# Kernel optimization log

Hardware: AMD Instinct MI355X
Metric: run time of the kernel (lower is better)

Reference implementation:

```python
import jax, jax.numpy as jnp
import numpy as np

B, T, C = 4, 2048, 2048
H, S = 32, 64
LN_EPS = 1e-5


def _layer_norm(x, w, b):
    mu = jnp.mean(x, axis=-1, keepdims=True)
    var = jnp.mean((x - mu) ** 2, axis=-1, keepdims=True)
    return (x - mu) / jnp.sqrt(var + LN_EPS) * w + b


def setup_inputs() -> dict:
    key = jax.random.key(0)
    ks = jax.random.split(key, 8)
    sc = 1.0 / np.sqrt(C)
    sc4 = 1.0 / np.sqrt(4 * C)
    return {
        "x": jax.random.normal(ks[0], (B, T, C), jnp.float32),
        "time_decay": jnp.full((H, S), -5.0, jnp.float32),
        "time_first": jnp.zeros((H, S), jnp.float32),
        "Wk": jax.random.normal(ks[1], (C, C), jnp.float32) * sc,
        "Wv": jax.random.normal(ks[2], (C, C), jnp.float32) * sc,
        "Wr": jax.random.normal(ks[3], (C, C), jnp.float32) * sc,
        "Wo": jax.random.normal(ks[4], (C, C), jnp.float32) * sc,
        "Wfk": jax.random.normal(ks[5], (C, 4 * C), jnp.float32) * sc,
        "Wfv": jax.random.normal(ks[6], (4 * C, C), jnp.float32) * sc4,
        "ln1_w": jnp.ones((C,), jnp.float32),
        "ln1_b": jnp.zeros((C,), jnp.float32),
        "ln2_w": jnp.ones((C,), jnp.float32),
        "ln2_b": jnp.zeros((C,), jnp.float32),
    }


def reference(x, time_decay, time_first, Wk, Wv, Wr, Wo, Wfk, Wfv,
              ln1_w, ln1_b, ln2_w, ln2_b):
    b, t, c = x.shape
    h, s = time_decay.shape
    xl = _layer_norm(x, ln1_w, ln1_b)
    k = (xl @ Wk).reshape(b, t, h, s)  # [B,T,H,S]
    v = (xl @ Wv).reshape(b, t, h, s)
    r = (xl @ Wr).reshape(b, t, h, s)

    decay = jnp.exp(-jnp.exp(time_decay))  # [H,S]
    u = jnp.exp(k) * v                      # [B,T,H,S]
    u_t = jnp.swapaxes(u, 0, 1)             # [T,B,H,S]

    def step(state, ut):
        state = decay * state + ut
        return state, state

    _, states = jax.lax.scan(step, jnp.zeros((b, h, s), x.dtype), u_t)  # [T,B,H,S]
    # t=0 bonus term: exp(time_first) * v_0 added to wkv only (not the state)
    states = states.at[0].add(jnp.exp(time_first) * v[:, 0])
    wkv = jnp.swapaxes(states, 0, 1)        # [B,T,H,S]

    rwkv = jax.nn.sigmoid(r) * wkv
    x = x + rwkv.reshape(b, t, c) @ Wo
    xl2 = _layer_norm(x, ln2_w, ln2_b)
    ffn = (jax.nn.relu(xl2 @ Wfk) ** 2) @ Wfv
    return x + ffn
```

## Files before the change

kernel.cpp:

```cpp
#include <hip/hip_runtime.h>
#include <hip/hip_bf16.h>
#include <stdint.h>

#define B_  4
#define T_  2048
#define C_  2048
#define H_  32
#define S_  64
#define M_  (B_ * T_)
#define C4_ (4 * C_)
#define C2_ (2 * C_)
#define LN_EPS 1e-5f
#define NCH 16
#define CLEN 128
#define NCHAN (B_ * C_)

typedef unsigned short u16;
typedef __attribute__((ext_vector_type(8))) short short8;
typedef __attribute__((ext_vector_type(4))) float f32x4;

__device__ __forceinline__ u16 f2bf(float f) {
  uint32_t u = __float_as_uint(f);
  u = (u + 0x7FFFu + ((u >> 16) & 1u)) >> 16;
  return (u16)u;
}
__device__ __forceinline__ float bf2f(u16 u) {
  return __uint_as_float(((uint32_t)u) << 16);
}

__device__ __forceinline__ void gload_lds16(const void* g, void* l) {
  __builtin_amdgcn_global_load_lds(
      (const __attribute__((address_space(1))) uint32_t*)g,
      (__attribute__((address_space(3))) uint32_t*)l, 16, 0, 0);
}

__global__ __launch_bounds__(256) void k_transpose_cast(
    const float* __restrict__ in, u16* __restrict__ out, int ld, int R, int Cn) {
  __shared__ float tile[32][33];
  const int tx = threadIdx.x & 31, ty = threadIdx.x >> 5;
  const int c0 = blockIdx.x * 32, r0 = blockIdx.y * 32;
#pragma unroll
  for (int i = 0; i < 4; ++i) {
    int r = ty + i * 8;
    tile[r][tx] = in[(size_t)(r0 + r) * ld + (c0 + tx)];
  }
  __syncthreads();
#pragma unroll
  for (int i = 0; i < 4; ++i) {
    int cc = ty + i * 8;
    out[(size_t)(c0 + cc) * R + (r0 + tx)] = f2bf(tile[tx][cc]);
  }
}

__global__ __launch_bounds__(256) void k_layernorm_bf16(
    const float* __restrict__ x, const float* __restrict__ w,
    const float* __restrict__ bias, u16* __restrict__ out) {
  const int row = blockIdx.x;
  const int t = threadIdx.x;
  const float* xr = x + (size_t)row * C_;
  float4 a = ((const float4*)xr)[2 * t];
  float4 b = ((const float4*)xr)[2 * t + 1];
  float s = a.x + a.y + a.z + a.w + b.x + b.y + b.z + b.w;
  float q = a.x * a.x + a.y * a.y + a.z * a.z + a.w * a.w +
            b.x * b.x + b.y * b.y + b.z * b.z + b.w * b.w;
#pragma unroll
  for (int off = 32; off > 0; off >>= 1) {
    s += __shfl_down(s, off);
    q += __shfl_down(q, off);
  }
  __shared__ float rs[8];
  const int wv = t >> 6;
  if ((t & 63) == 0) { rs[wv] = s; rs[4 + wv] = q; }
  __syncthreads();
  s = rs[0] + rs[1] + rs[2] + rs[3];
  q = rs[4] + rs[5] + rs[6] + rs[7];
  const float mean = s * (1.0f / C_);
  const float rstd = rsqrtf(q * (1.0f / C_) - mean * mean + LN_EPS);
  float4 w0 = ((const float4*)w)[2 * t], w1 = ((const float4*)w)[2 * t + 1];
  float4 b0 = ((const float4*)bias)[2 * t], b1 = ((const float4*)bias)[2 * t + 1];
  uint4 pk;
  pk.x = (uint32_t)f2bf((a.x - mean) * rstd * w0.x + b0.x) |
         ((uint32_t)f2bf((a.y - mean) * rstd * w0.y + b0.y) << 16);
  pk.y = (uint32_t)f2bf((a.z - mean) * rstd * w0.z + b0.z) |
         ((uint32_t)f2bf((a.w - mean) * rstd * w0.w + b0.w) << 16);
  pk.z = (uint32_t)f2bf((b.x - mean) * rstd * w1.x + b1.x) |
         ((uint32_t)f2bf((b.y - mean) * rstd * w1.y + b1.y) << 16);
  pk.w = (uint32_t)f2bf((b.z - mean) * rstd * w1.z + b1.z) |
         ((uint32_t)f2bf((b.w - mean) * rstd * w1.w + b1.w) << 16);
  ((uint4*)(out + (size_t)row * C_))[t] = pk;
}

__device__ __forceinline__ void stage_half(
    const u16* __restrict__ G, int ldK, int row0, int kcol0,
    u16* lds_half, int tid) {
#pragma unroll
  for (int i = 0; i < 2; ++i) {
    const int slot = i * 512 + tid;
    const int row = slot >> 2;
    const int gs = slot & 3;
    const int gsrc = gs ^ ((row >> 1) & 3);
    gload_lds16(G + (size_t)(row0 + row) * ldK + kcol0 + gsrc * 8,
                ((char*)lds_half) + i * 8192 + (tid >> 6) * 1024);
  }
}

__device__ __forceinline__ short8 frag(const u16* half_base, int row, int g0) {
  const int g = g0 ^ ((row >> 1) & 3);
  return *(const short8*)(half_base + row * 32 + g * 8);
}

template <int EPI>
__global__ __launch_bounds__(512, 2) void k_gemm8(
    const u16* __restrict__ A, const u16* __restrict__ Bt,
    void* __restrict__ Out, const float* __restrict__ Res,
    int M, int N, int K) {
  __shared__ u16 As[2][2][256 * 32];
  __shared__ u16 Bs[2][2][256 * 32];
  const int tid = threadIdx.x;
  const int wv = tid >> 6, ln = tid & 63;
  const int wm = wv >> 2, wn = wv & 3;
  const int l15 = ln & 15, g0 = ln >> 4;

  const int lin = blockIdx.y * gridDim.x + blockIdx.x;
  const int xcd = lin & 7, slot = lin >> 3;
  const int bx = slot % gridDim.x;
  const int by = xcd * (gridDim.y >> 3) + slot / gridDim.x;
  const int bm0 = by * 256, bn0 = bx * 256;
  const int NT = K >> 6;

  f32x4 acc[8][4];
#pragma unroll
  for (int m = 0; m < 8; ++m)
#pragma unroll
    for (int n = 0; n < 4; ++n) acc[m][n] = (f32x4)0.0f;

  stage_half(A, K, bm0, 0, &As[0][0][0], tid);
  stage_half(Bt, K, bn0, 0, &Bs[0][0][0], tid);
  stage_half(A, K, bm0, 32, &As[0][1][0], tid);
  stage_half(Bt, K, bn0, 32, &Bs[0][1][0], tid);
  asm volatile("s_waitcnt vmcnt(4)" ::: "memory");
  __builtin_amdgcn_s_barrier();
  __builtin_amdgcn_sched_barrier(0);

  for (int t = 0; t < NT; ++t) {
    const int c = t & 1, nb = c ^ 1;
    const int kn = (t + 1) << 6;
    const bool stage_on = (t + 1 < NT);
    const bool lastt = (t + 1 == NT);
    short8 bfr[4], af[4];

#pragma unroll
    for (int h = 0; h < 2; ++h) {
#pragma unroll
      for (int n = 0; n < 4; ++n)
        bfr[n] = frag(&Bs[c][h][0], wn * 64 + n * 16 + l15, g0);
#pragma unroll
      for (int m = 0; m < 4; ++m)
        af[m] = frag(&As[c][h][0], wm * 128 + m * 16 + l15, g0);
      if (stage_on) stage_half(A, K, bm0, kn + h * 32, &As[nb][h][0], tid);
#pragma unroll
      for (int m = 0; m < 4; ++m)
#pragma unroll
        for (int n = 0; n < 4; ++n)
          acc[m][n] = __builtin_amdgcn_mfma_f32_16x16x32_bf16(af[m], bfr[n], acc[m][n], 0, 0, 0);

#pragma unroll
      for (int m = 0; m < 4; ++m)
        af[m] = frag(&As[c][h][0], wm * 128 + 64 + m * 16 + l15, g0);
      if (stage_on) stage_half(Bt, K, bn0, kn + h * 32, &Bs[nb][h][0], tid);
#pragma unroll
      for (int m = 0; m < 4; ++m)
#pragma unroll
        for (int n = 0; n < 4; ++n)
          acc[4 + m][n] = __builtin_amdgcn_mfma_f32_16x16x32_bf16(af[m], bfr[n], acc[4 + m][n], 0, 0, 0);

      if (h == 0) {
        if (!lastt) asm volatile("s_waitcnt vmcnt(4)" ::: "memory");
        else        asm volatile("s_waitcnt vmcnt(0)" ::: "memory");
        __builtin_amdgcn_s_barrier();
        __builtin_amdgcn_sched_barrier(0);
      } else if (!lastt) {
        asm volatile("s_waitcnt vmcnt(4)" ::: "memory");
        __builtin_amdgcn_s_barrier();
        __builtin_amdgcn_sched_barrier(0);
      }
    }
  }

#pragma unroll
  for (int m = 0; m < 8; ++m) {
    const int r_base = bm0 + wm * 128 + m * 16 + (ln >> 4) * 4;
#pragma unroll
    for (int n = 0; n < 4; ++n) {
      const int cidx = bn0 + wn * 64 + n * 16 + l15;
#pragma unroll
      for (int i = 0; i < 4; ++i) {
        const size_t off = (size_t)(r_base + i) * N + cidx;
        const float v = acc[m][n][i];
        if constexpr (EPI == 0) {
          ((float*)Out)[off] = v;
        } else if constexpr (EPI == 1) {
          ((float*)Out)[off] = Res[off] + v;
        } else if constexpr (EPI == 2) {
          ((u16*)Out)[off] = f2bf(v);
        } else if constexpr (EPI == 3) {
          const float tpos = v > 0.0f ? v : 0.0f;
          ((u16*)Out)[off] = f2bf(tpos * tpos);
        } else {
          ((float*)Out)[off] += v;
        }
      }
    }
  }
}

__global__ __launch_bounds__(256) void k_scan_a(
    const float* __restrict__ kk, const u16* __restrict__ vv,
    const float* __restrict__ td, float* __restrict__ Sloc) {
  const int g = blockIdx.x * 256 + threadIdx.x;
  const int j = blockIdx.y;
  const int ch = g & (C_ - 1);
  const float d = __expf(-__expf(td[ch]));
  const size_t base = ((size_t)(g >> 11) * T_ + (size_t)j * CLEN) * C_ + ch;
  float s = 0.0f;
#pragma unroll 4
  for (int t = 0; t < CLEN; ++t) {
    const size_t idx = base + (size_t)t * C_;
    s = d * s + __expf(kk[idx]) * bf2f(vv[idx]);
  }
  Sloc[(size_t)j * NCHAN + g] = s;
}

__global__ __launch_bounds__(256) void k_scan_b(
    const float* __restrict__ td, const float* __restrict__ Sloc,
    float* __restrict__ carry) {
  const int g = blockIdx.x * 256 + threadIdx.x;
  const int ch = g & (C_ - 1);
  const float dL = __expf(-__expf(td[ch]) * (float)CLEN);
  float s = 0.0f;
#pragma unroll
  for (int j = 0; j < NCH; ++j) {
    carry[(size_t)j * NCHAN + g] = s;
    s = dL * s + Sloc[(size_t)j * NCHAN + g];
  }
}

__global__ __launch_bounds__(256) void k_scan_c(
    const float* __restrict__ kk, const u16* __restrict__ vv,
    const u16* __restrict__ rr, const float* __restrict__ td,
    const float* __restrict__ tf, const float* __restrict__ carry,
    u16* __restrict__ rwkv) {
  const int g = blockIdx.x * 256 + threadIdx.x;
  const int j = blockIdx.y;
  const int ch = g & (C_ - 1);
  const float d = __expf(-__expf(td[ch]));
  const float bonus = __expf(tf[ch]);
  const size_t base = ((size_t)(g >> 11) * T_ + (size_t)j * CLEN) * C_ + ch;
  float s = carry[(size_t)j * NCHAN + g];
#pragma unroll 2
  for (int t = 0; t < CLEN; ++t) {
    const size_t idx = base + (size_t)t * C_;
    const float vval = bf2f(vv[idx]);
    s = d * s + __expf(kk[idx]) * vval;
    float wkv = s;
    if (j == 0 && t == 0) wkv += bonus * vval;
    const float rv = bf2f(rr[idx]);
    const float sg = 1.0f / (1.0f + __expf(-rv));
    rwkv[idx] = f2bf(sg * wkv);
  }
}

extern "C" void kernel_launch(void* const* d_in, const int* in_sizes, int n_in,
                              void* d_out, int out_size, void* d_ws, size_t ws_size,
                              hipStream_t stream) {
  const float* x    = (const float*)d_in[0];
  const float* td   = (const float*)d_in[1];
  const float* tf   = (const float*)d_in[2];
  const float* Wk   = (const float*)d_in[3];
  const float* Wv   = (const float*)d_in[4];
  const float* Wr   = (const float*)d_in[5];
  const float* Wo   = (const float*)d_in[6];
  const float* Wfk  = (const float*)d_in[7];
  const float* Wfv  = (const float*)d_in[8];
  const float* ln1w = (const float*)d_in[9];
  const float* ln1b = (const float*)d_in[10];
  const float* ln2w = (const float*)d_in[11];
  const float* ln2b = (const float*)d_in[12];
  float* out = (float*)d_out;

  char* p = (char*)d_ws;
  auto alloc = [&](size_t bytes) {
    char* r = p;
    p += (bytes + 255) & ~(size_t)255;
    return r;
  };
  u16*   wbuf = (u16*)alloc((size_t)C_ * C_ * 2);
  u16*   xl   = (u16*)alloc((size_t)M_ * C_ * 2);
  float* kbuf = (float*)alloc((size_t)M_ * C_ * 4);
  u16*   vbuf = (u16*)alloc((size_t)M_ * C_ * 2);
  u16*   rbuf = (u16*)alloc((size_t)M_ * C_ * 2);
  float* Sloc = (float*)alloc((size_t)NCH * NCHAN * 4);
  float* carry = (float*)alloc((size_t)NCH * NCHAN * 4);
  u16* rwkv = rbuf;
  u16* hchunk = xl;
  u16* wfbuf = rbuf;

  const dim3 tgrid(C_ / 32, C_ / 32);
  const dim3 ggrid(C_ / 256, M_ / 256);

  k_layernorm_bf16<<<M_, 256, 0, stream>>>(x, ln1w, ln1b, xl);

  k_transpose_cast<<<tgrid, 256, 0, stream>>>(Wk, wbuf, C_, C_, C_);
  k_gemm8<0><<<ggrid, 512, 0, stream>>>(xl, wbuf, kbuf, nullptr, M_, C_, C_);
  k_transpose_cast<<<tgrid, 256, 0, stream>>>(Wv, wbuf, C_, C_, C_);
  k_gemm8<2><<<ggrid, 512, 0, stream>>>(xl, wbuf, vbuf, nullptr, M_, C_, C_);
  k_transpose_cast<<<tgrid, 256, 0, stream>>>(Wr, wbuf, C_, C_, C_);
  k_gemm8<2><<<ggrid, 512, 0, stream>>>(xl, wbuf, rbuf, nullptr, M_, C_, C_);

  k_scan_a<<<dim3(NCHAN / 256, NCH), 256, 0, stream>>>(kbuf, vbuf, td, Sloc);
  k_scan_b<<<dim3(NCHAN / 256), 256, 0, stream>>>(td, Sloc, carry);
  k_scan_c<<<dim3(NCHAN / 256, NCH), 256, 0, stream>>>(kbuf, vbuf, rbuf, td, tf, carry, rwkv);

  k_transpose_cast<<<tgrid, 256, 0, stream>>>(Wo, wbuf, C_, C_, C_);
  k_gemm8<1><<<ggrid, 512, 0, stream>>>(rwkv, wbuf, out, x, M_, C_, C_);

  u16* xl2 = vbuf;
  k_layernorm_bf16<<<M_, 256, 0, stream>>>(out, ln2w, ln2b, xl2);

  for (int c = 0; c < 2; ++c) {
    k_transpose_cast<<<dim3(C2_ / 32, C_ / 32), 256, 0, stream>>>(
        Wfk + (size_t)c * C2_, wfbuf, C4_, C_, C2_);
    k_gemm8<3><<<dim3(C2_ / 256, M_ / 256), 512, 0, stream>>>(
        xl2, wfbuf, hchunk, nullptr, M_, C2_, C_);
    k_transpose_cast<<<dim3(C_ / 32, C2_ / 32), 256, 0, stream>>>(
        Wfv + (size_t)c * C2_ * C_, wfbuf, C_, C2_, C_);
    k_gemm8<4><<<dim3(C_ / 256, M_ / 256), 512, 0, stream>>>(
        hchunk, wfbuf, out, nullptr, M_, C_, C2_);
  }
}
```

Baseline: 955.6 us.

## Shrink GEMM tile to 256x128 with K=32 steps and higher occupancy

Replaces the 256x256, K-64 double-buffered GEMM with a 256x128 tile that steps K by 32, uses 4x4 accumulators per wave, and requests 4 blocks per CU. This cuts LDS and register use so more blocks can be resident and latency is hidden by occupancy rather than intra-block pipelining. In exchange each tile has lower arithmetic intensity, there is a full barrier with vmcnt(0) every 32-wide K step, and the grid doubles in size.

```diff
diff --git a/kernel.cpp b/kernel.cpp
--- a/kernel.cpp
+++ b/kernel.cpp
@@ -90,106 +90,91 @@
   ((uint4*)(out + (size_t)row * C_))[t] = pk;
 }
 
-__device__ __forceinline__ void stage_half(
-    const u16* __restrict__ G, int ldK, int row0, int kcol0,
-    u16* lds_half, int tid) {
-#pragma unroll
-  for (int i = 0; i < 2; ++i) {
-    const int slot = i * 512 + tid;
-    const int row = slot >> 2;
-    const int gs = slot & 3;
-    const int gsrc = gs ^ ((row >> 1) & 3);
-    gload_lds16(G + (size_t)(row0 + row) * ldK + kcol0 + gsrc * 8,
-                ((char*)lds_half) + i * 8192 + (tid >> 6) * 1024);
-  }
-}
-
-__device__ __forceinline__ short8 frag(const u16* half_base, int row, int g0) {
+__device__ __forceinline__ short8 frag(const u16* buf_base, int row, int g0) {
   const int g = g0 ^ ((row >> 1) & 3);
-  return *(const short8*)(half_base + row * 32 + g * 8);
+  return *(const short8*)(buf_base + row * 32 + g * 8);
 }
 
 template <int EPI>
-__global__ __launch_bounds__(512, 2) void k_gemm8(
+__global__ __launch_bounds__(512, 4) void k_gemm2(
     const u16* __restrict__ A, const u16* __restrict__ Bt,
     void* __restrict__ Out, const float* __restrict__ Res,
     int M, int N, int K) {
-  __shared__ u16 As[2][2][256 * 32];
-  __shared__ u16 Bs[2][2][256 * 32];
+  __shared__ u16 As[2][256 * 32];
+  __shared__ u16 Bs[2][128 * 32];
   const int tid = threadIdx.x;
   const int wv = tid >> 6, ln = tid & 63;
-  const int wm = wv >> 2, wn = wv & 3;
+  const int wm = wv >> 1, wn = wv & 1;
   const int l15 = ln & 15, g0 = ln >> 4;
 
   const int lin = blockIdx.y * gridDim.x + blockIdx.x;
   const int xcd = lin & 7, slot = lin >> 3;
   const int bx = slot % gridDim.x;
   const int by = xcd * (gridDim.y >> 3) + slot / gridDim.x;
-  const int bm0 = by * 256, bn0 = bx * 256;
-  const int NT = K >> 6;
-
-  f32x4 acc[8][4];
-#pragma unroll
-  for (int m = 0; m < 8; ++m)
+  const int bm0 = by * 256, bn0 = bx * 128;
+  const int NT = K >> 5;
+
+  const int arow = tid >> 2, ag = tid & 3;
+  const int agsrc0 = ag ^ ((arow >> 1) & 3);
+  const int agsrc1 = ag ^ (((arow + 128) >> 1) & 3);
+  const int brow = tid >> 2, bg = tid & 3;
+  const int bgsrc = bg ^ ((brow >> 1) & 3);
+
+  f32x4 acc[4][4];
+#pragma unroll
+  for (int m = 0; m < 4; ++m)
 #pragma unroll
     for (int n = 0; n < 4; ++n) acc[m][n] = (f32x4)0.0f;
 
-  stage_half(A, K, bm0, 0, &As[0][0][0], tid);
-  stage_half(Bt, K, bn0, 0, &Bs[0][0][0], tid);
-  stage_half(A, K, bm0, 32, &As[0][1][0], tid);
-  stage_half(Bt, K, bn0, 32, &Bs[0][1][0], tid);
-  asm volatile("s_waitcnt vmcnt(4)" ::: "memory");
+  gload_lds16(A + (size_t)(bm0 + arow) * K + agsrc0 * 8,
+              ((char*)&As[0][0]) + wv * 1024);
+  gload_lds16(A + (size_t)(bm0 + 128 + arow) * K + agsrc1 * 8,
+              ((char*)&As[0][0]) + 8192 + wv * 1024);
+  gload_lds16(Bt + (size_t)(bn0 + brow) * K + bgsrc * 8,
+              ((char*)&Bs[0][0]) + wv * 1024);
+  asm volatile("s_waitcnt vmcnt(0)" ::: "memory");
   __builtin_amdgcn_s_barrier();
   __builtin_amdgcn_sched_barrier(0);
 
   for (int t = 0; t < NT; ++t) {
     const int c = t & 1, nb = c ^ 1;
-    const int kn = (t + 1) << 6;
+    const int kn = (t + 1) << 5;
     const bool stage_on = (t + 1 < NT);
-    const bool lastt = (t + 1 == NT);
-    short8 bfr[4], af[4];
-
-#pragma unroll
-    for (int h = 0; h < 2; ++h) {
+    short8 af[4], bfr[4];
+
+#pragma unroll
+    for (int m = 0; m < 4; ++m)
+      af[m] = frag(&As[c][0], wm * 64 + m * 16 + l15, g0);
+#pragma unroll
+    for (int n = 0; n < 4; ++n)
+      bfr[n] = frag(&Bs[c][0], wn * 64 + n * 16 + l15, g0);
+
+    if (stage_on) {
+      gload_lds16(A + (size_t)(bm0 + arow) * K + kn + agsrc0 * 8,
+                  ((char*)&As[nb][0]) + wv * 1024);
+      gload_lds16(A + (size_t)(bm0 + 128 + arow) * K + kn + agsrc1 * 8,
+                  ((char*)&As[nb][0]) + 8192 + wv * 1024);
+      gload_lds16(Bt + (size_t)(bn0 + brow) * K + kn + bgsrc * 8,
+                  ((char*)&Bs[nb][0]) + wv * 1024);
+    }
+
+#pragma unroll
+    for (int m = 0; m < 4; ++m)
 #pragma unroll
       for (int n = 0; n < 4; ++n)
-        bfr[n] = frag(&Bs[c][h][0], wn * 64 + n * 16 + l15, g0);
-#pragma unroll
-      for (int m = 0; m < 4; ++m)
-        af[m] = frag(&As[c][h][0], wm * 128 + m * 16 + l15, g0);
-      if (stage_on) stage_half(A, K, bm0, kn + h * 32, &As[nb][h][0], tid);
-#pragma unroll
-      for (int m = 0; m < 4; ++m)
-#pragma unroll
-        for (int n = 0; n < 4; ++n)
-          acc[m][n] = __builtin_amdgcn_mfma_f32_16x16x32_bf16(af[m], bfr[n], acc[m][n], 0, 0, 0);
-
-#pragma unroll
-      for (int m = 0; m < 4; ++m)
-        af[m] = frag(&As[c][h][0], wm * 128 + 64 + m * 16 + l15, g0);
-      if (stage_on) stage_half(Bt, K, bn0, kn + h * 32, &Bs[nb][h][0], tid);
-#pragma unroll
-      for (int m = 0; m < 4; ++m)
-#pragma unroll
-        for (int n = 0; n < 4; ++n)
-          acc[4 + m][n] = __builtin_amdgcn_mfma_f32_16x16x32_bf16(af[m], bfr[n], acc[4 + m][n], 0, 0, 0);
-
-      if (h == 0) {
-        if (!lastt) asm volatile("s_waitcnt vmcnt(4)" ::: "memory");
-        else        asm volatile("s_waitcnt vmcnt(0)" ::: "memory");
-        __builtin_amdgcn_s_barrier();
-        __builtin_amdgcn_sched_barrier(0);
-      } else if (!lastt) {
-        asm volatile("s_waitcnt vmcnt(4)" ::: "memory");
-        __builtin_amdgcn_s_barrier();
-        __builtin_amdgcn_sched_barrier(0);
-      }
+        acc[m][n] = __builtin_amdgcn_mfma_f32_16x16x32_bf16(af[m], bfr[n], acc[m][n], 0, 0, 0);
+
+    if (stage_on) {
+      __builtin_amdgcn_sched_barrier(0);
+      asm volatile("s_waitcnt vmcnt(0) lgkmcnt(0)" ::: "memory");
+      __builtin_amdgcn_s_barrier();
+      __builtin_amdgcn_sched_barrier(0);
     }
   }
 
 #pragma unroll
-  for (int m = 0; m < 8; ++m) {
-    const int r_base = bm0 + wm * 128 + m * 16 + (ln >> 4) * 4;
+  for (int m = 0; m < 4; ++m) {
+    const int r_base = bm0 + wm * 64 + m * 16 + g0 * 4;
 #pragma unroll
     for (int n = 0; n < 4; ++n) {
       const int cidx = bn0 + wn * 64 + n * 16 + l15;
@@ -306,23 +291,23 @@
   u16* wfbuf = rbuf;
 
   const dim3 tgrid(C_ / 32, C_ / 32);
-  const dim3 ggrid(C_ / 256, M_ / 256);
+  const dim3 ggrid(C_ / 128, M_ / 256);
 
   k_layernorm_bf16<<<M_, 256, 0, stream>>>(x, ln1w, ln1b, xl);
 
   k_transpose_cast<<<tgrid, 256, 0, stream>>>(Wk, wbuf, C_, C_, C_);
-  k_gemm8<0><<<ggrid, 512, 0, stream>>>(xl, wbuf, kbuf, nullptr, M_, C_, C_);
+  k_gemm2<0><<<ggrid, 512, 0, stream>>>(xl, wbuf, kbuf, nullptr, M_, C_, C_);
   k_transpose_cast<<<tgrid, 256, 0, stream>>>(Wv, wbuf, C_, C_, C_);
-  k_gemm8<2><<<ggrid, 512, 0, stream>>>(xl, wbuf, vbuf, nullptr, M_, C_, C_);
+  k_gemm2<2><<<ggrid, 512, 0, stream>>>(xl, wbuf, vbuf, nullptr, M_, C_, C_);
   k_transpose_cast<<<tgrid, 256, 0, stream>>>(Wr, wbuf, C_, C_, C_);
-  k_gemm8<2><<<ggrid, 512, 0, stream>>>(xl, wbuf, rbuf, nullptr, M_, C_, C_);
+  k_gemm2<2><<<ggrid, 512, 0, stream>>>(xl, wbuf, rbuf, nullptr, M_, C_, C_);
 
   k_scan_a<<<dim3(NCHAN / 256, NCH), 256, 0, stream>>>(kbuf, vbuf, td, Sloc);
   k_scan_b<<<dim3(NCHAN / 256), 256, 0, stream>>>(td, Sloc, carry);
   k_scan_c<<<dim3(NCHAN / 256, NCH), 256, 0, stream>>>(kbuf, vbuf, rbuf, td, tf, carry, rwkv);
 
   k_transpose_cast<<<tgrid, 256, 0, stream>>>(Wo, wbuf, C_, C_, C_);
-  k_gemm8<1><<<ggrid, 512, 0, stream>>>(rwkv, wbuf, out, x, M_, C_, C_);
+  k_gemm2<1><<<ggrid, 512, 0, stream>>>(rwkv, wbuf, out, x, M_, C_, C_);
 
   u16* xl2 = vbuf;
   k_layernorm_bf16<<<M_, 256, 0, stream>>>(out, ln2w, ln2b, xl2);
@@ -330,11 +315,11 @@
   for (int c = 0; c < 2; ++c) {
     k_transpose_cast<<<dim3(C2_ / 32, C_ / 32), 256, 0, stream>>>(
         Wfk + (size_t)c * C2_, wfbuf, C4_, C_, C2_);
-    k_gemm8<3><<<dim3(C2_ / 256, M_ / 256), 512, 0, stream>>>(
+    k_gemm2<3><<<dim3(C2_ / 128, M_ / 256), 512, 0, stream>>>(
         xl2, wfbuf, hchunk, nullptr, M_, C2_, C_);
     k_transpose_cast<<<dim3(C_ / 32, C2_ / 32), 256, 0, stream>>>(
         Wfv + (size_t)c * C2_ * C_, wfbuf, C_, C2_, C_);
-    k_gemm8<4><<<dim3(C_ / 256, M_ / 256), 512, 0, stream>>>(
+    k_gemm2<4><<<dim3(C_ / 128, M_ / 256), 512, 0, stream>>>(
         hchunk, wfbuf, out, nullptr, M_, C_, C2_);
   }
 }
```

After: 1.037 ms. +8.6%, slower.
